# Kernel tuning notes

Hardware: AMD Instinct MI355X
Metric: run time of the kernel (lower is better)

Reference implementation:

```python
import jax, jax.numpy as jnp
import numpy as np

B, N, E = 128, 100, 800          # graphs, nodes/graph, edges/graph
TN, TE = B * N, B * E
NODE_EMB, REL_EMB, H = 128, 256, 256   # hidden_size == relation_emb in CoMPILE
R, DEPTH = 200, 3
EDGE_EMB = 2 * NODE_EMB + REL_EMB      # 512


def _gru_dir(x, h0, w_ih, w_hh, b_ih, b_hh):
    """One direction of a torch-style GRU. x: [B,T,H], h0: [B,H] -> [B,T,H]."""
    def step(h, xt):
        gi = xt @ w_ih.T + b_ih
        gh = h @ w_hh.T + b_hh
        i_r, i_z, i_n = jnp.split(gi, 3, axis=-1)
        h_r, h_z, h_n = jnp.split(gh, 3, axis=-1)
        r = jax.nn.sigmoid(i_r + h_r)
        z = jax.nn.sigmoid(i_z + h_z)
        n = jnp.tanh(i_n + r * h_n)
        hn = (1.0 - z) * n + z * h
        return hn, hn
    _, ys = jax.lax.scan(step, h0, jnp.swapaxes(x, 0, 1))
    return jnp.swapaxes(ys, 0, 1)


def setup_inputs() -> dict:
    key = jax.random.key(0)
    ks = iter(jax.random.split(key, 40))
    def w(shape):
        return jax.random.normal(next(ks), shape, jnp.float32) * 0.05
    inp = {}
    inp["node_feat"] = jax.random.normal(next(ks), (TN, NODE_EMB), jnp.float32)
    inp["rel_emb"] = jax.random.normal(next(ks), (R, REL_EMB), jnp.float32)  # final_relation_embeddings
    # model weights (bias=False everywhere except W_o, linear1, gru)
    inp["W_i_node"] = w((H, NODE_EMB))
    inp["W_i_edge"] = w((H, EDGE_EMB))
    inp["Wa1"] = w((H, 2 * H))          # input_attention1
    inp["Wa2"] = w((1, H))              # input_attention2
    inp["W_h_atom"] = w((DEPTH - 1, H, H))
    inp["W_h_bond"] = w((DEPTH - 1, H, H))
    inp["Wd1"] = w((DEPTH - 1, H, H + REL_EMB))  # Attention1_d
    inp["Wd2"] = w((DEPTH - 1, 1, H))            # Attention2_d
    inp["W_comm"] = w((H, 3 * H))       # communicate_mlp
    inp["gru_bias"] = w((H,))
    inp["w_ih_f"] = w((3 * H, H)); inp["w_hh_f"] = w((3 * H, H))
    inp["b_ih_f"] = w((3 * H,));   inp["b_hh_f"] = w((3 * H,))
    inp["w_ih_b"] = w((3 * H, H)); inp["w_hh_b"] = w((3 * H, H))
    inp["b_ih_b"] = w((3 * H,));   inp["b_hh_b"] = w((3 * H,))
    inp["W_o"] = w((H, 2 * H)); inp["b_o"] = w((H,))
    inp["W_lin1"] = w((1, H)); inp["b_lin1"] = w((1,))
    # graph structure: edges stay inside their own subgraph (block-diagonal batching)
    off = (jnp.arange(B, dtype=jnp.int64)[:, None] * N)
    inp["edge_src"] = (jax.random.randint(next(ks), (B, E), 0, N) + off).reshape(-1)
    inp["edge_dst"] = (jax.random.randint(next(ks), (B, E), 0, N) + off).reshape(-1)
    inp["edge_rel"] = jax.random.randint(next(ks), (TE,), 0, R)
    inp["batch_rel"] = jax.random.randint(next(ks), (B,), 0, R)
    inp["src_node"] = jax.random.randint(next(ks), (B,), 0, N) + jnp.arange(B) * N
    inp["tgt_node"] = jax.random.randint(next(ks), (B,), 0, N) + jnp.arange(B) * N
    return inp


def reference(node_feat, rel_emb, W_i_node, W_i_edge, Wa1, Wa2, W_h_atom, W_h_bond,
              Wd1, Wd2, W_comm, gru_bias, w_ih_f, w_hh_f, b_ih_f, b_hh_f,
              w_ih_b, w_hh_b, b_ih_b, b_hh_b, W_o, b_o, W_lin1, b_lin1,
              edge_src, edge_dst, edge_rel, batch_rel, src_node, tgt_node):
    act = jax.nn.relu  # args.activation = 'ReLU'
    tgt_rel = rel_emb[batch_rel]                              # [B,H] per-query relation
    e_rel = rel_emb[edge_rel]                                 # [TE,H]
    edge_feat = jnp.concatenate([node_feat[edge_src], e_rel, node_feat[edge_dst]], 1)  # [TE,EDGE_EMB]
    input_node = act(node_feat @ W_i_node.T)                  # [TN,H]
    message_node = input_node
    input_edge = act(edge_feat @ W_i_edge.T)                  # [TE,H]
    message_edge = input_edge
    edge_tgt_rel = jnp.repeat(tgt_rel, E, axis=0)             # [TE,H] target relation per edge
    total_source = jnp.repeat(src_node, E)                    # [TE] query head node per edge
    total_target = jnp.repeat(tgt_node, E)
    # input edge attention vs translational query embedding
    g_edge = message_node[total_source] + edge_tgt_rel - message_node[total_target]
    att = jnp.tanh(jnp.concatenate([message_edge, g_edge], 1) @ Wa1.T)
    att = jax.nn.sigmoid(att @ Wa2.T)
    message_edge = message_edge * att
    for d in range(DEPTH - 1):
        # edge->node aggregation (MySpMM with target-side incidence e2n_sp)
        agg = jax.ops.segment_sum(message_edge, edge_dst, num_segments=TN)
        message_node = act((message_node + agg) @ W_h_atom[d].T)
        # node->edge (e2n_sp2^T: gather source-node states per edge)
        message_edge = act(input_edge + message_node[edge_src] @ W_h_bond[d].T)
        att = jnp.tanh(jnp.concatenate([message_edge, edge_tgt_rel], 1) @ Wd1[d].T)
        att = jax.nn.sigmoid(att @ Wd2[d].T)
        message_edge = message_edge * att
    agg = jax.ops.segment_sum(message_edge, edge_dst, num_segments=TN)
    agg2 = jnp.concatenate([agg, message_node, input_node], 1) @ W_comm.T  # [TN,H]
    # BatchGRU: uniform graph sizes -> pad/unpad is a reshape
    msg = act(agg2 + gru_bias).reshape(B, N, H)
    h0 = agg2.reshape(B, N, H).max(axis=1)                    # per-graph max of hidden
    out_f = _gru_dir(msg, h0, w_ih_f, w_hh_f, b_ih_f, b_hh_f)
    out_b = _gru_dir(msg[:, ::-1], h0, w_ih_b, w_hh_b, b_ih_b, b_hh_b)[:, ::-1]
    a_message = act(jnp.concatenate([out_f, out_b], -1).reshape(TN, 2 * H))
    atom_h = act(a_message @ W_o.T + b_o)                     # [TN,H]
    conv = jnp.tanh(atom_h[src_node] + tgt_rel - atom_h[tgt_node])  # [B,H]
    return conv @ W_lin1.T + b_lin1                           # [B,1]
```

## Files before the change

### kernel.cpp

```cpp
#include <hip/hip_runtime.h>
#include <cstddef>

#define Bg 128
#define Nn 100
#define Eg 800
#define TNODE 12800
#define TEDGE 102400
#define HD 256
#define NEMB 128
#define REMB 256

typedef short bf8 __attribute__((ext_vector_type(8)));
typedef short bf4 __attribute__((ext_vector_type(4)));
typedef float f4  __attribute__((ext_vector_type(4)));

__device__ __forceinline__ float relu_(float x){ return x > 0.f ? x : 0.f; }
__device__ __forceinline__ float sigm_(float x){ return 1.f/(1.f + __expf(-x)); }
__device__ __forceinline__ float4 ld4(const float* p){ return *(const float4*)p; }
__device__ __forceinline__ void st4(float* p, float4 v){ *(float4*)p = v; }
__device__ __forceinline__ float4 add4(float4 a, float4 b){
    return float4{a.x+b.x, a.y+b.y, a.z+b.z, a.w+b.w};
}
__device__ __forceinline__ float4 relu4(float4 a){
    return float4{relu_(a.x), relu_(a.y), relu_(a.z), relu_(a.w)};
}
__device__ __forceinline__ short f2bf(float f){
    unsigned u = __float_as_uint(f);
    u += 0x7fff + ((u >> 16) & 1);
    return (short)(u >> 16);
}
__device__ __forceinline__ float bf2f(short s){
    return __uint_as_float(((unsigned)(unsigned short)s) << 16);
}
__device__ __forceinline__ void split4(float4 v, bf4& h, bf4& l){
    h.x = f2bf(v.x); l.x = f2bf(v.x - bf2f(h.x));
    h.y = f2bf(v.y); l.y = f2bf(v.y - bf2f(h.y));
    h.z = f2bf(v.z); l.z = f2bf(v.z - bf2f(h.z));
    h.w = f2bf(v.w); l.w = f2bf(v.w - bf2f(h.w));
}
__device__ __forceinline__ f4 mfma_(bf8 a, bf8 b, f4 c){
    return __builtin_amdgcn_mfma_f32_16x16x32_bf16(a, b, c, 0, 0, 0);
}

enum { A_PLAIN=0, A_ADD=1, A_RELUB=2, A_CLAMP=3, A_CAT3=4, A_CAT2R=5 };
enum { E_STORE=0, E_RELU=1, E_BIAS=2, E_BIASRELU=3 };

template<int AM, int EM>
__global__ __launch_bounds__(256, 2)
void mgemm(const float* __restrict__ A0, const float* __restrict__ A1,
           const float* __restrict__ A2, const float* __restrict__ W,
           const float* __restrict__ bias, float* __restrict__ C,
           int M, int N, int K, int lda, int wld)
{
    __shared__ short Ah[128][40], Al[128][40], Bh[128][40], Bl[128][40];
    const int t  = threadIdx.x;
    const int kc = t & 7, lr = t >> 3;
    const int lane = t & 63, wv = t >> 6;
    const int wm = wv >> 1, wn = wv & 1;
    const int frow = lane & 15, fk = (lane >> 4) * 8;
    const int row0 = blockIdx.y * 128, col0 = blockIdx.x * 128;

    f4 acc[4][4] = {};

    for (int k0 = 0; k0 < K; k0 += 32) {
        const int gk = k0 + kc * 4;
        const int kk = kc * 4;
        #pragma unroll
        for (int ri = 0; ri < 4; ri++) {
            int row = lr + 32 * ri;
            int grow = row0 + row;
            float4 v;
            if (AM == A_PLAIN) {
                v = ld4(A0 + (size_t)grow * lda + gk);
            } else if (AM == A_ADD) {
                v = add4(ld4(A0 + (size_t)grow * lda + gk),
                         ld4(A1 + (size_t)grow * lda + gk));
            } else if (AM == A_RELUB) {
                v = relu4(add4(ld4(A0 + (size_t)grow * lda + gk), ld4(A1 + gk)));
            } else if (AM == A_CLAMP) {
                int cr = grow < M ? grow : M - 1;
                v = ld4(A0 + (size_t)cr * lda + gk);
            } else if (AM == A_CAT3) {
                if (gk < HD)        v = ld4(A0 + (size_t)grow * HD + gk);
                else if (gk < 2*HD) v = ld4(A1 + (size_t)grow * HD + gk - HD);
                else                v = ld4(A2 + (size_t)grow * HD + gk - 2*HD);
            } else {
                v = (gk < HD) ? relu4(ld4(A0 + (size_t)grow * HD + gk))
                              : relu4(ld4(A1 + (size_t)grow * HD + gk - HD));
            }
            bf4 h, l; split4(v, h, l);
            *(bf4*)&Ah[row][kk] = h;
            *(bf4*)&Al[row][kk] = l;
        }
        #pragma unroll
        for (int ri = 0; ri < 4; ri++) {
            int wr = lr + 32 * ri;
            float4 v = ld4(W + (size_t)(col0 + wr) * wld + gk);
            bf4 h, l; split4(v, h, l);
            *(bf4*)&Bh[wr][kk] = h;
            *(bf4*)&Bl[wr][kk] = l;
        }
        __syncthreads();
        bf8 ah[4], al[4], bh[4], bl[4];
        #pragma unroll
        for (int mi = 0; mi < 4; mi++) {
            ah[mi] = *(const bf8*)&Ah[wm*64 + mi*16 + frow][fk];
            al[mi] = *(const bf8*)&Al[wm*64 + mi*16 + frow][fk];
        }
        #pragma unroll
        for (int ni = 0; ni < 4; ni++) {
            bh[ni] = *(const bf8*)&Bh[wn*64 + ni*16 + frow][fk];
            bl[ni] = *(const bf8*)&Bl[wn*64 + ni*16 + frow][fk];
        }
        #pragma unroll
        for (int mi = 0; mi < 4; mi++)
            #pragma unroll
            for (int ni = 0; ni < 4; ni++) {
                acc[mi][ni] = mfma_(ah[mi], bh[ni], acc[mi][ni]);
                acc[mi][ni] = mfma_(ah[mi], bl[ni], acc[mi][ni]);
                acc[mi][ni] = mfma_(al[mi], bh[ni], acc[mi][ni]);
            }
        __syncthreads();
    }
    #pragma unroll
    for (int mi = 0; mi < 4; mi++) {
        #pragma unroll
        for (int ni = 0; ni < 4; ni++) {
            int ccol = col0 + wn*64 + ni*16 + frow;
            int rbase = row0 + wm*64 + mi*16 + (lane >> 4) * 4;
            #pragma unroll
            for (int reg = 0; reg < 4; reg++) {
                float v = acc[mi][ni][reg];
                if (EM == E_BIAS || EM == E_BIASRELU) v += bias[ccol];
                if (EM == E_RELU || EM == E_BIASRELU) v = relu_(v);
                C[(size_t)(rbase + reg) * N + ccol] = v;
            }
        }
    }
}

template<int MODE>
__global__ __launch_bounds__(256, 2)
void mattn(const float* __restrict__ S, const float* __restrict__ Rt,
           const float* __restrict__ D, const float* __restrict__ T0,
           const int* __restrict__ esrc, const int* __restrict__ erel,
           const int* __restrict__ edst,
           const float* __restrict__ W1, const float* __restrict__ W2,
           const float* __restrict__ term, float* __restrict__ sbuf)
{
    __shared__ short Ah[64][40], Al[64][40], Bh[256][40], Bl[256][40];
    __shared__ float partl[4][64];
    __shared__ int isrc[64], irel[64], idst[64];
    const int t = threadIdx.x;
    const int kc = t & 7, lr = t >> 3;
    const int lane = t & 63, wv = t >> 6;
    const int frow = lane & 15, fk = (lane >> 4) * 8;
    const int r0 = blockIdx.x * 64;

    if (t < 64) {
        int e = r0 + t;
        isrc[t] = esrc[e]; irel[t] = erel[e]; idst[t] = edst[e];
    }
    __syncthreads();

    f4 acc[4][4] = {};

    for (int k0 = 0; k0 < HD; k0 += 32) {
        const int gk = k0 + kc * 4;
        const int kk = kc * 4;
        #pragma unroll
        for (int ri = 0; ri < 2; ri++) {
            int row = lr + 32 * ri;
            int s = isrc[row], rl = irel[row], dd = idst[row];
            float4 v = relu4(add4(add4(ld4(S + (size_t)s * HD + gk),
                                       ld4(Rt + (size_t)rl * HD + gk)),
                                  ld4(D + (size_t)dd * HD + gk)));
            if (MODE) v = relu4(add4(v, ld4(T0 + (size_t)s * HD + gk)));
            bf4 h, l; split4(v, h, l);
            *(bf4*)&Ah[row][kk] = h;
            *(bf4*)&Al[row][kk] = l;
        }
        #pragma unroll
        for (int ri = 0; ri < 8; ri++) {
            int wr = lr + 32 * ri;
            float4 v = ld4(W1 + (size_t)wr * 512 + gk);
            bf4 h, l; split4(v, h, l);
            *(bf4*)&Bh[wr][kk] = h;
            *(bf4*)&Bl[wr][kk] = l;
        }
        __syncthreads();
        bf8 ah[4], al[4], bh[4], bl[4];
        #pragma unroll
        for (int mi = 0; mi < 4; mi++) {
            ah[mi] = *(const bf8*)&Ah[mi*16 + frow][fk];
            al[mi] = *(const bf8*)&Al[mi*16 + frow][fk];
        }
        #pragma unroll
        for (int ni = 0; ni < 4; ni++) {
            bh[ni] = *(const bf8*)&Bh[wv*64 + ni*16 + frow][fk];
            bl[ni] = *(const bf8*)&Bl[wv*64 + ni*16 + frow][fk];
        }
        #pragma unroll
        for (int mi = 0; mi < 4; mi++)
            #pragma unroll
            for (int ni = 0; ni < 4; ni++) {
                acc[mi][ni] = mfma_(ah[mi], bh[ni], acc[mi][ni]);
                acc[mi][ni] = mfma_(ah[mi], bl[ni], acc[mi][ni]);
                acc[mi][ni] = mfma_(al[mi], bh[ni], acc[mi][ni]);
            }
        __syncthreads();
    }
    #pragma unroll
    for (int mi = 0; mi < 4; mi++) {
        #pragma unroll
        for (int reg = 0; reg < 4; reg++) {
            int rl = mi*16 + (lane >> 4) * 4 + reg;
            int g = (r0 + rl) / Eg;
            float p = 0.f;
            #pragma unroll
            for (int ni = 0; ni < 4; ni++) {
                int n = wv*64 + ni*16 + frow;
                p += tanhf(acc[mi][ni][reg] + term[g*HD + n]) * W2[n];
            }
            p += __shfl_xor(p, 1); p += __shfl_xor(p, 2);
            p += __shfl_xor(p, 4); p += __shfl_xor(p, 8);
            if (frow == 0) partl[wv][rl] = p;
        }
    }
    __syncthreads();
    if (t < 64) {
        float p = partl[0][t] + partl[1][t] + partl[2][t] + partl[3][t];
        sbuf[r0 + t] = sigm_(p);
    }
}

template<int MODE>
__global__ __launch_bounds__(256)
void agg_gather(const float* __restrict__ S, const float* __restrict__ Rt,
                const float* __restrict__ D, const float* __restrict__ T0,
                const int* __restrict__ esrc, const int* __restrict__ erel,
                const int* __restrict__ rowptr, const int* __restrict__ eidx,
                const float* __restrict__ s, float* __restrict__ agg)
{
    int node = blockIdx.x * 4 + (threadIdx.x >> 6);
    int c = (threadIdx.x & 63) * 4;
    float4 dn = ld4(D + (size_t)node * HD + c);
    float4 acc{0.f, 0.f, 0.f, 0.f};
    int beg = rowptr[node], end = rowptr[node + 1];
    for (int i = beg; i < end; i++) {
        int e = eidx[i];
        int sr = esrc[e], rl = erel[e];
        float4 v = relu4(add4(add4(ld4(S + (size_t)sr * HD + c),
                                   ld4(Rt + (size_t)rl * HD + c)), dn));
        if (MODE) v = relu4(add4(v, ld4(T0 + (size_t)sr * HD + c)));
        float sc = s[e];
        acc.x += v.x * sc; acc.y += v.y * sc;
        acc.z += v.z * sc; acc.w += v.w * sc;
    }
    st4(agg + (size_t)node * HD + c, acc);
}

__global__ void zeroi_kernel(int* __restrict__ p)
{
    p[blockIdx.x * 256 + threadIdx.x] = 0;
}
__global__ void csr_count(const int* __restrict__ dst, int* __restrict__ cnt)
{
    int e = blockIdx.x * 256 + threadIdx.x;
    atomicAdd(&cnt[dst[e]], 1);
}
__global__ void csr_scan(const int* __restrict__ cnt, int* __restrict__ rowptr)
{
    __shared__ int ws[4];
    __shared__ int carry;
    int tid = threadIdx.x;
    if (tid == 0) carry = 0;
    __syncthreads();
    for (int i = 0; i < TNODE; i += 256) {
        int v = cnt[i + tid];
        int x = v;
        #pragma unroll
        for (int off = 1; off < 64; off <<= 1) {
            int y = __shfl_up(x, off);
            if ((tid & 63) >= off) x += y;
        }
        if ((tid & 63) == 63) ws[tid >> 6] = x;
        __syncthreads();
        int add = carry;
        int w = tid >> 6;
        for (int j = 0; j < w; j++) add += ws[j];
        rowptr[i + tid] = add + x - v;
        __syncthreads();
        if (tid == 255) carry = add + x;
        __syncthreads();
    }
    if (tid == 0) rowptr[TNODE] = carry;
}
__global__ void csr_fill(const int* __restrict__ dst, const int* __restrict__ rowptr,
                         int* __restrict__ fillc, int* __restrict__ eidx)
{
    int e = blockIdx.x * 256 + threadIdx.x;
    int d = dst[e];
    int slot = rowptr[d] + atomicAdd(&fillc[d], 1);
    eidx[slot] = e;
}

__global__ __launch_bounds__(256)
void term_kernel(const float* __restrict__ mn, const float* __restrict__ tgt_rel,
                 const float* __restrict__ Wa1, const float* __restrict__ Wd1,
                 const int* __restrict__ srcn, const int* __restrict__ tgtn,
                 float* __restrict__ term)
{
    __shared__ float Gs[HD];
    int b = blockIdx.x % Bg;
    int which = blockIdx.x / Bg;
    int c = threadIdx.x;
    float g;
    if (which == 0)
        g = mn[(size_t)srcn[b]*HD + c] + tgt_rel[b*HD + c] - mn[(size_t)tgtn[b]*HD + c];
    else
        g = tgt_rel[b*HD + c];
    Gs[c] = g;
    __syncthreads();
    const float* W = (which == 0) ? Wa1 : (Wd1 + (size_t)(which-1)*HD*512);
    float p = 0.f;
    for (int k = 0; k < HD; k += 4) {
        float4 w = ld4(W + (size_t)c*512 + 256 + k);
        p = fmaf(Gs[k], w.x, p); p = fmaf(Gs[k+1], w.y, p);
        p = fmaf(Gs[k+2], w.z, p); p = fmaf(Gs[k+3], w.w, p);
    }
    term[(size_t)which*Bg*HD + b*HD + c] = p;
}

__global__ void tgtrel_kernel(const float* __restrict__ rel_emb, const int* __restrict__ batch_rel,
                              float* __restrict__ tgt_rel)
{
    int b = blockIdx.x, c = threadIdx.x;
    tgt_rel[b*HD + c] = rel_emb[(size_t)batch_rel[b]*REMB + c];
}

__global__ void h0_kernel(const float* __restrict__ agg2, float* __restrict__ h0)
{
    int b = blockIdx.x, c = threadIdx.x;
    float m = -1e30f;
    for (int n = 0; n < Nn; n++)
        m = fmaxf(m, agg2[((size_t)b*Nn + n)*HD + c]);
    h0[b*HD + c] = m;
}

__global__ void whbf_kernel(const float* __restrict__ whf, const float* __restrict__ whb,
                            short* __restrict__ whbf)
{
    int idx = blockIdx.x * 256 + threadIdx.x;
    int d = idx / (768*256), rem = idx % (768*256);
    whbf[idx] = f2bf((d ? whb : whf)[rem]);
}

__global__ __launch_bounds__(512, 2)
void gru_seq(const float* __restrict__ gi_f, const float* __restrict__ gi_b,
             const short* __restrict__ whbf,
             const float* __restrict__ bhf, const float* __restrict__ bhb,
             const float* __restrict__ h0,
             float* __restrict__ outf, float* __restrict__ outb)
{
    __shared__ float hsf[16][260];
    __shared__ short hsh[16][264];
    __shared__ short hsl[16][264];
    __shared__ float gates[768][17];
    __shared__ float bsh[768];
    const int blk = blockIdx.x;
    const int d = blk >> 3, grp = blk & 7;
    const int tid = threadIdx.x;
    const int lane = tid & 63, wv = tid >> 6;
    const int f16 = lane & 15;
    const int kb  = (lane >> 4) * 8;

    const short* wp0 = whbf + (size_t)d * 768 * 256;
    const float* gi  = d ? gi_b : gi_f;
    const float* bh  = d ? bhb : bhf;
    float* outp      = d ? outb : outf;

    for (int i = tid; i < 768; i += 512) bsh[i] = bh[i];

    bf8 wreg[6][8];
    #pragma unroll
    for (int j = 0; j < 6; j++) {
        int wr = (wv*6 + j) * 16 + f16;
        const short* wp = wp0 + (size_t)wr * 256 + kb;
        #pragma unroll
        for (int ks = 0; ks < 8; ks++)
            wreg[j][ks] = *(const bf8*)(wp + ks*32);
    }

    const int eseq = tid >> 5, ehb = tid & 31;
    {
        #pragma unroll
        for (int hh = 0; hh < 8; hh++) {
            int h = ehb + hh * 32;
            float v = h0[(size_t)(grp*16 + eseq) * HD + h];
            hsf[eseq][h] = v;
            short hi = f2bf(v);
            hsh[eseq][h] = hi;
            hsl[eseq][h] = f2bf(v - bf2f(hi));
        }
    }
    __syncthreads();

    for (int t = 0; t < Nn; t++) {
        int trow = d ? (Nn - 1 - t) : t;
        float gr[8], gz[8], gn[8];
        {
            size_t girow = ((size_t)(grp*16 + eseq) * Nn + trow) * 768;
            #pragma unroll
            for (int hh = 0; hh < 8; hh++) {
                int h = ehb + hh * 32;
                gr[hh] = gi[girow + h];
                gz[hh] = gi[girow + 256 + h];
                gn[hh] = gi[girow + 512 + h];
            }
        }
        #pragma unroll
        for (int j = 0; j < 6; j++) {
            f4 acc = {};
            #pragma unroll
            for (int ks = 0; ks < 8; ks++) {
                bf8 ahi = *(const bf8*)&hsh[f16][ks*32 + kb];
                bf8 alo = *(const bf8*)&hsl[f16][ks*32 + kb];
                acc = mfma_(ahi, wreg[j][ks], acc);
                acc = mfma_(alo, wreg[j][ks], acc);
            }
            #pragma unroll
            for (int reg = 0; reg < 4; reg++)
                gates[(wv*6 + j)*16 + f16][(lane >> 4)*4 + reg] = acc[reg];
        }
        __syncthreads();
        {
            size_t orow = ((size_t)(grp*16 + eseq) * Nn + trow) * HD;
            #pragma unroll
            for (int hh = 0; hh < 8; hh++) {
                int h = ehb + hh * 32;
                float R  = gates[h][eseq];
                float Z  = gates[256 + h][eseq];
                float NN = gates[512 + h][eseq];
                float hprev = hsf[eseq][h];
                float r = sigm_(gr[hh] + R + bsh[h]);
                float z = sigm_(gz[hh] + Z + bsh[256 + h]);
                float n = tanhf(gn[hh] + r * (NN + bsh[512 + h]));
                float nh = (1.f - z) * n + z * hprev;
                hsf[eseq][h] = nh;
                short hi = f2bf(nh);
                hsh[eseq][h] = hi;
                hsl[eseq][h] = f2bf(nh - bf2f(hi));
                outp[orow + h] = nh;
            }
        }
        __syncthreads();
    }
}

__global__ __launch_bounds__(256)
void final_kernel(const float* __restrict__ atom_h, const float* __restrict__ tgt_rel,
                  const int* __restrict__ srcn, const int* __restrict__ tgtn,
                  const float* __restrict__ Wl, const float* __restrict__ bl,
                  float* __restrict__ out)
{
    __shared__ float red[4];
    int b = blockIdx.x, c = threadIdx.x;
    float v = tanhf(atom_h[(size_t)srcn[b]*HD + c] + tgt_rel[b*HD + c]
                    - atom_h[(size_t)tgtn[b]*HD + c]);
    float p = v * Wl[c];
    #pragma unroll
    for (int off = 1; off < 64; off <<= 1) p += __shfl_xor(p, off);
    int wv = c >> 6;
    if ((c & 63) == 0) red[wv] = p;
    __syncthreads();
    if (c == 0) out[b] = red[0] + red[1] + red[2] + red[3] + bl[0];
}

extern "C" void kernel_launch(void* const* d_in, const int* in_sizes, int n_in,
                              void* d_out, int out_size, void* d_ws, size_t ws_size,
                              hipStream_t stream)
{
    const float* node_feat = (const float*)d_in[0];
    const float* rel_emb   = (const float*)d_in[1];
    const float* W_i_node  = (const float*)d_in[2];
    const float* W_i_edge  = (const float*)d_in[3];
    const float* Wa1       = (const float*)d_in[4];
    const float* Wa2       = (const float*)d_in[5];
    const float* W_h_atom  = (const float*)d_in[6];
    const float* W_h_bond  = (const float*)d_in[7];
    const float* Wd1       = (const float*)d_in[8];
    const float* Wd2       = (const float*)d_in[9];
    const float* W_comm    = (const float*)d_in[10];
    const float* gru_bias  = (const float*)d_in[11];
    const float* w_ih_f    = (const float*)d_in[12];
    const float* w_hh_f    = (const float*)d_in[13];
    const float* b_ih_f    = (const float*)d_in[14];
    const float* b_hh_f    = (const float*)d_in[15];
    const float* w_ih_b    = (const float*)d_in[16];
    const float* w_hh_b    = (const float*)d_in[17];
    const float* b_ih_b    = (const float*)d_in[18];
    const float* b_hh_b    = (const float*)d_in[19];
    const float* W_o       = (const float*)d_in[20];
    const float* b_o       = (const float*)d_in[21];
    const float* W_lin1    = (const float*)d_in[22];
    const float* b_lin1    = (const float*)d_in[23];
    const int* edge_src  = (const int*)d_in[24];
    const int* edge_dst  = (const int*)d_in[25];
    const int* edge_rel  = (const int*)d_in[26];
    const int* batch_rel = (const int*)d_in[27];
    const int* src_node  = (const int*)d_in[28];
    const int* tgt_node  = (const int*)d_in[29];
    float* out = (float*)d_out;

    float* ws = (float*)d_ws;
    size_t off = 0;
    auto alloc = [&](size_t n){ float* p = ws + off; off += n; return p; };
    float* tgt_rel    = alloc((size_t)Bg*HD);
    float* term       = alloc((size_t)3*Bg*HD);
    float* input_node = alloc((size_t)TNODE*HD);
    float* mn_a       = alloc((size_t)TNODE*HD);
    float* mn_b       = alloc((size_t)TNODE*HD);
    float* agg        = alloc((size_t)TNODE*HD);
    float* h0v        = alloc((size_t)Bg*HD);
    short* whbf       = (short*)alloc((size_t)2*768*256/2);
    float* sbuf       = alloc((size_t)TEDGE);
    int*   cnt        = (int*)alloc((size_t)TNODE);
    int*   fillc      = (int*)alloc((size_t)TNODE);
    int*   rowptr     = (int*)alloc((size_t)TNODE + 256);
    int*   eidx       = (int*)alloc((size_t)TEDGE);
    float* Sbuf       = alloc((size_t)TNODE*HD);
    float* Dbuf       = alloc((size_t)TNODE*HD);
    float* Rbuf       = alloc((size_t)256*HD);
    float* gi_f       = alloc((size_t)TNODE*768);
    float* gi_b       = alloc((size_t)TNODE*768);
    float* out_f      = alloc((size_t)TNODE*HD);
    float* out_b      = alloc((size_t)TNODE*HD);
    float* agg2   = mn_a;
    float* atom_h = input_node;

    tgtrel_kernel<<<Bg, 256, 0, stream>>>(rel_emb, batch_rel, tgt_rel);
    whbf_kernel<<<1536, 256, 0, stream>>>(w_hh_f, w_hh_b, whbf);

    zeroi_kernel<<<2*TNODE/256, 256, 0, stream>>>(cnt);
    csr_count<<<TEDGE/256, 256, 0, stream>>>(edge_dst, cnt);
    csr_scan<<<1, 256, 0, stream>>>(cnt, rowptr);
    csr_fill<<<TEDGE/256, 256, 0, stream>>>(edge_dst, rowptr, fillc, eidx);

    mgemm<A_PLAIN, E_RELU><<<dim3(HD/128, TNODE/128), 256, 0, stream>>>(
        node_feat, nullptr, nullptr, W_i_node, nullptr, input_node,
        TNODE, HD, NEMB, NEMB, NEMB);

    mgemm<A_PLAIN, E_STORE><<<dim3(HD/128, TNODE/128), 256, 0, stream>>>(
        node_feat, nullptr, nullptr, W_i_edge + 0, nullptr, Sbuf,
        TNODE, HD, NEMB, NEMB, 512);
    mgemm<A_PLAIN, E_STORE><<<dim3(HD/128, TNODE/128), 256, 0, stream>>>(
        node_feat, nullptr, nullptr, W_i_edge + 384, nullptr, Dbuf,
        TNODE, HD, NEMB, NEMB, 512);
    mgemm<A_CLAMP, E_STORE><<<dim3(HD/128, 2), 256, 0, stream>>>(
        rel_emb, nullptr, nullptr, W_i_edge + 128, nullptr, Rbuf,
        200, HD, REMB, REMB, 512);

    term_kernel<<<3*Bg, 256, 0, stream>>>(input_node, tgt_rel, Wa1, Wd1,
                                          src_node, tgt_node, term);

    mattn<0><<<TEDGE/64, 256, 0, stream>>>(Sbuf, Rbuf, Dbuf, Sbuf,
        edge_src, edge_rel, edge_dst, Wa1, Wa2, term, sbuf);
    agg_gather<0><<<TNODE/4, 256, 0, stream>>>(Sbuf, Rbuf, Dbuf, Sbuf,
        edge_src, edge_rel, rowptr, eidx, sbuf, agg);

    const float* mn_cur = input_node;
    float* bufs[2] = {mn_a, mn_b};
    for (int d = 0; d < 2; d++) {
        float* mn_next = bufs[d];
        float* tmp     = bufs[1-d];
        mgemm<A_ADD, E_RELU><<<dim3(2, TNODE/128), 256, 0, stream>>>(
            mn_cur, agg, nullptr, W_h_atom + (size_t)d*HD*HD, nullptr, mn_next,
            TNODE, HD, HD, HD, HD);
        mgemm<A_PLAIN, E_STORE><<<dim3(2, TNODE/128), 256, 0, stream>>>(
            mn_next, nullptr, nullptr, W_h_bond + (size_t)d*HD*HD, nullptr, tmp,
            TNODE, HD, HD, HD, HD);
        mattn<1><<<TEDGE/64, 256, 0, stream>>>(Sbuf, Rbuf, Dbuf, tmp,
            edge_src, edge_rel, edge_dst, Wd1 + (size_t)d*HD*512,
            Wd2 + (size_t)d*HD, term + (size_t)(1+d)*Bg*HD, sbuf);
        agg_gather<1><<<TNODE/4, 256, 0, stream>>>(Sbuf, Rbuf, Dbuf, tmp,
            edge_src, edge_rel, rowptr, eidx, sbuf, agg);
        mn_cur = mn_next;
    }

    mgemm<A_CAT3, E_STORE><<<dim3(2, TNODE/128), 256, 0, stream>>>(
        agg, (const float*)mn_cur, input_node, W_comm, nullptr, agg2,
        TNODE, HD, 3*HD, 0, 3*HD);

    h0_kernel<<<Bg, 256, 0, stream>>>(agg2, h0v);

    mgemm<A_RELUB, E_BIAS><<<dim3(768/128, TNODE/128), 256, 0, stream>>>(
        agg2, gru_bias, nullptr, w_ih_f, b_ih_f, gi_f,
        TNODE, 768, HD, HD, HD);
    mgemm<A_RELUB, E_BIAS><<<dim3(768/128, TNODE/128), 256, 0, stream>>>(
        agg2, gru_bias, nullptr, w_ih_b, b_ih_b, gi_b,
        TNODE, 768, HD, HD, HD);

    gru_seq<<<16, 512, 0, stream>>>(gi_f, gi_b, whbf, b_hh_f, b_hh_b, h0v,
                                    out_f, out_b);

    mgemm<A_CAT2R, E_BIASRELU><<<dim3(2, TNODE/128), 256, 0, stream>>>(
        out_f, out_b, nullptr, W_o, b_o, atom_h,
        TNODE, HD, 2*HD, 0, 2*HD);

    final_kernel<<<Bg, 256, 0, stream>>>(atom_h, tgt_rel, src_node, tgt_node,
                                         W_lin1, b_lin1, out);
}
```

Measured before the change: 1.478 ms.

## Restructure GRU recurrence to 4 waves with more register-held weights and folded biases

The sequential GRU kernel now runs 256 threads per block instead of 512, so each wave keeps 12 weight tiles in registers and interleaves four independent MFMA accumulators to hide MFMA latency. The r/z hidden biases are folded into the input-gate GEMM bias through a small new kernel, and the n-gate hidden bias is kept in registers, which removes the shared bias table. Input-gate loads move after the barrier and become float4 vector loads, as do the output stores. The trade-off is fewer waves per block, higher register pressure, and less latency hiding for the global gate loads.

```diff
diff --git a/kernel.cpp b/kernel.cpp
--- a/kernel.cpp
+++ b/kernel.cpp
@@ -356,7 +356,18 @@
     whbf[idx] = f2bf((d ? whb : whf)[rem]);
 }
 
-__global__ __launch_bounds__(512, 2)
+__global__ void biascomb_kernel(const float* __restrict__ bihf, const float* __restrict__ bhhf,
+                                const float* __restrict__ bihb, const float* __restrict__ bhhb,
+                                float* __restrict__ bc)
+{
+    int i = blockIdx.x * 256 + threadIdx.x;
+    int d = i / 768, r = i % 768;
+    const float* bi = d ? bihb : bihf;
+    const float* bhh = d ? bhhb : bhhf;
+    bc[i] = bi[r] + (r < 512 ? bhh[r] : 0.f);
+}
+
+__global__ __launch_bounds__(256, 1)
 void gru_seq(const float* __restrict__ gi_f, const float* __restrict__ gi_b,
              const short* __restrict__ whbf,
              const float* __restrict__ bhf, const float* __restrict__ bhb,
@@ -367,7 +378,6 @@
     __shared__ short hsh[16][264];
     __shared__ short hsl[16][264];
     __shared__ float gates[768][17];
-    __shared__ float bsh[768];
     const int blk = blockIdx.x;
     const int d = blk >> 3, grp = blk & 7;
     const int tid = threadIdx.x;
@@ -380,23 +390,26 @@
     const float* bh  = d ? bhb : bhf;
     float* outp      = d ? outb : outf;
 
-    for (int i = tid; i < 768; i += 512) bsh[i] = bh[i];
-
-    bf8 wreg[6][8];
+    bf8 wreg[12][8];
     #pragma unroll
-    for (int j = 0; j < 6; j++) {
-        int wr = (wv*6 + j) * 16 + f16;
+    for (int j = 0; j < 12; j++) {
+        int wr = (wv*12 + j) * 16 + f16;
         const short* wp = wp0 + (size_t)wr * 256 + kb;
         #pragma unroll
         for (int ks = 0; ks < 8; ks++)
             wreg[j][ks] = *(const bf8*)(wp + ks*32);
     }
 
-    const int eseq = tid >> 5, ehb = tid & 31;
+    const int eseq = tid >> 4;
+    const int eh0  = (tid & 15) * 16;
+    float bhn[16];
+    #pragma unroll
+    for (int hh = 0; hh < 16; hh++) bhn[hh] = bh[512 + eh0 + hh];
+
     {
         #pragma unroll
-        for (int hh = 0; hh < 8; hh++) {
-            int h = ehb + hh * 32;
+        for (int hh = 0; hh < 16; hh++) {
+            int h = eh0 + hh;
             float v = h0[(size_t)(grp*16 + eseq) * HD + h];
             hsf[eseq][h] = v;
             short hi = f2bf(v);
@@ -408,50 +421,64 @@
 
     for (int t = 0; t < Nn; t++) {
         int trow = d ? (Nn - 1 - t) : t;
-        float gr[8], gz[8], gn[8];
-        {
-            size_t girow = ((size_t)(grp*16 + eseq) * Nn + trow) * 768;
-            #pragma unroll
-            for (int hh = 0; hh < 8; hh++) {
-                int h = ehb + hh * 32;
-                gr[hh] = gi[girow + h];
-                gz[hh] = gi[girow + 256 + h];
-                gn[hh] = gi[girow + 512 + h];
-            }
-        }
-        #pragma unroll
-        for (int j = 0; j < 6; j++) {
-            f4 acc = {};
+        #pragma unroll
+        for (int g = 0; g < 3; g++) {
+            f4 acc0 = {}, acc1 = {}, acc2 = {}, acc3 = {};
             #pragma unroll
             for (int ks = 0; ks < 8; ks++) {
                 bf8 ahi = *(const bf8*)&hsh[f16][ks*32 + kb];
                 bf8 alo = *(const bf8*)&hsl[f16][ks*32 + kb];
-                acc = mfma_(ahi, wreg[j][ks], acc);
-                acc = mfma_(alo, wreg[j][ks], acc);
-            }
+                acc0 = mfma_(ahi, wreg[g*4+0][ks], acc0);
+                acc1 = mfma_(ahi, wreg[g*4+1][ks], acc1);
+                acc2 = mfma_(ahi, wreg[g*4+2][ks], acc2);
+                acc3 = mfma_(ahi, wreg[g*4+3][ks], acc3);
+                acc0 = mfma_(alo, wreg[g*4+0][ks], acc0);
+                acc1 = mfma_(alo, wreg[g*4+1][ks], acc1);
+                acc2 = mfma_(alo, wreg[g*4+2][ks], acc2);
+                acc3 = mfma_(alo, wreg[g*4+3][ks], acc3);
+            }
+            int rb = (wv*12 + g*4) * 16 + f16;
+            int cb = (lane >> 4) * 4;
             #pragma unroll
-            for (int reg = 0; reg < 4; reg++)
-                gates[(wv*6 + j)*16 + f16][(lane >> 4)*4 + reg] = acc[reg];
+            for (int reg = 0; reg < 4; reg++) {
+                gates[rb +  0][cb + reg] = acc0[reg];
+                gates[rb + 16][cb + reg] = acc1[reg];
+                gates[rb + 32][cb + reg] = acc2[reg];
+                gates[rb + 48][cb + reg] = acc3[reg];
+            }
         }
         __syncthreads();
         {
-            size_t orow = ((size_t)(grp*16 + eseq) * Nn + trow) * HD;
+            size_t girow = ((size_t)(grp*16 + eseq) * Nn + trow) * 768;
+            size_t orow  = ((size_t)(grp*16 + eseq) * Nn + trow) * HD;
             #pragma unroll
-            for (int hh = 0; hh < 8; hh++) {
-                int h = ehb + hh * 32;
-                float R  = gates[h][eseq];
-                float Z  = gates[256 + h][eseq];
-                float NN = gates[512 + h][eseq];
-                float hprev = hsf[eseq][h];
-                float r = sigm_(gr[hh] + R + bsh[h]);
-                float z = sigm_(gz[hh] + Z + bsh[256 + h]);
-                float n = tanhf(gn[hh] + r * (NN + bsh[512 + h]));
-                float nh = (1.f - z) * n + z * hprev;
-                hsf[eseq][h] = nh;
-                short hi = f2bf(nh);
-                hsh[eseq][h] = hi;
-                hsl[eseq][h] = f2bf(nh - bf2f(hi));
-                outp[orow + h] = nh;
+            for (int c2 = 0; c2 < 4; c2++) {
+                int hb = eh0 + c2*4;
+                float4 g_r = ld4(gi + girow + hb);
+                float4 g_z = ld4(gi + girow + 256 + hb);
+                float4 g_n = ld4(gi + girow + 512 + hb);
+                float4 onew;
+                #pragma unroll
+                for (int e = 0; e < 4; e++) {
+                    int h = hb + e;
+                    float R  = gates[h][eseq];
+                    float Z  = gates[256 + h][eseq];
+                    float NN = gates[512 + h][eseq];
+                    float hprev = hsf[eseq][h];
+                    float gre = ((const float*)&g_r)[e];
+                    float gze = ((const float*)&g_z)[e];
+                    float gne = ((const float*)&g_n)[e];
+                    float r = sigm_(gre + R);
+                    float z = sigm_(gze + Z);
+                    float n = tanhf(gne + r * (NN + bhn[c2*4 + e]));
+                    float nh = (1.f - z) * n + z * hprev;
+                    hsf[eseq][h] = nh;
+                    short hi = f2bf(nh);
+                    hsh[eseq][h] = hi;
+                    hsl[eseq][h] = f2bf(nh - bf2f(hi));
+                    ((float*)&onew)[e] = nh;
+                }
+                st4(outp + orow + hb, onew);
             }
         }
         __syncthreads();
@@ -524,6 +551,7 @@
     float* agg        = alloc((size_t)TNODE*HD);
     float* h0v        = alloc((size_t)Bg*HD);
     short* whbf       = (short*)alloc((size_t)2*768*256/2);
+    float* bcomb      = alloc((size_t)2*768);
     float* sbuf       = alloc((size_t)TEDGE);
     int*   cnt        = (int*)alloc((size_t)TNODE);
     int*   fillc      = (int*)alloc((size_t)TNODE);
@@ -541,6 +569,7 @@
 
     tgtrel_kernel<<<Bg, 256, 0, stream>>>(rel_emb, batch_rel, tgt_rel);
     whbf_kernel<<<1536, 256, 0, stream>>>(w_hh_f, w_hh_b, whbf);
+    biascomb_kernel<<<6, 256, 0, stream>>>(b_ih_f, b_hh_f, b_ih_b, b_hh_b, bcomb);
 
     zeroi_kernel<<<2*TNODE/256, 256, 0, stream>>>(cnt);
     csr_count<<<TEDGE/256, 256, 0, stream>>>(edge_dst, cnt);
@@ -595,13 +624,13 @@
     h0_kernel<<<Bg, 256, 0, stream>>>(agg2, h0v);
 
     mgemm<A_RELUB, E_BIAS><<<dim3(768/128, TNODE/128), 256, 0, stream>>>(
-        agg2, gru_bias, nullptr, w_ih_f, b_ih_f, gi_f,
+        agg2, gru_bias, nullptr, w_ih_f, bcomb, gi_f,
         TNODE, 768, HD, HD, HD);
     mgemm<A_RELUB, E_BIAS><<<dim3(768/128, TNODE/128), 256, 0, stream>>>(
-        agg2, gru_bias, nullptr, w_ih_b, b_ih_b, gi_b,
+        agg2, gru_bias, nullptr, w_ih_b, bcomb + 768, gi_b,
         TNODE, 768, HD, HD, HD);
 
-    gru_seq<<<16, 512, 0, stream>>>(gi_f, gi_b, whbf, b_hh_f, b_hh_b, h0v,
+    gru_seq<<<16, 256, 0, stream>>>(gi_f, gi_b, whbf, b_hh_f, b_hh_b, h0v,
                                     out_f, out_b);
 
     mgemm<A_CAT2R, E_BIASRELU><<<dim3(2, TNODE/128), 256, 0, stream>>>(
```

Result: slower. 1.799 ms (+21.8%).

## Fold GRU hidden biases into input GEMM and halve register-resident recurrent weights

Applied to the files above, without the earlier changes.

Precomputes combined r/z biases (b_ih + b_hh) and passes them to the input-projection GEMM epilogue, so the sequential GRU kernel no longer stages biases in shared memory and keeps only the n-gate hidden bias in registers. It also keeps just half of the recurrent weight fragments in registers and reloads the other half from global memory (L2/L1) on every timestep. This lowers register pressure in the latency-bound recurrent loop, but adds global loads to each step of the serial chain.

```diff
diff --git a/kernel.cpp b/kernel.cpp
--- a/kernel.cpp
+++ b/kernel.cpp
@@ -356,6 +356,17 @@
     whbf[idx] = f2bf((d ? whb : whf)[rem]);
 }
 
+__global__ void biascomb_kernel(const float* __restrict__ bihf, const float* __restrict__ bhhf,
+                                const float* __restrict__ bihb, const float* __restrict__ bhhb,
+                                float* __restrict__ bc)
+{
+    int i = blockIdx.x * 256 + threadIdx.x;
+    int d = i / 768, r = i % 768;
+    const float* bi = d ? bihb : bihf;
+    const float* bhh = d ? bhhb : bhhf;
+    bc[i] = bi[r] + (r < 512 ? bhh[r] : 0.f);
+}
+
 __global__ __launch_bounds__(512, 2)
 void gru_seq(const float* __restrict__ gi_f, const float* __restrict__ gi_b,
              const short* __restrict__ whbf,
@@ -367,7 +378,6 @@
     __shared__ short hsh[16][264];
     __shared__ short hsl[16][264];
     __shared__ float gates[768][17];
-    __shared__ float bsh[768];
     const int blk = blockIdx.x;
     const int d = blk >> 3, grp = blk & 7;
     const int tid = threadIdx.x;
@@ -380,19 +390,21 @@
     const float* bh  = d ? bhb : bhf;
     float* outp      = d ? outb : outf;
 
-    for (int i = tid; i < 768; i += 512) bsh[i] = bh[i];
-
-    bf8 wreg[6][8];
+    bf8 wregA[3][8];
     #pragma unroll
-    for (int j = 0; j < 6; j++) {
+    for (int j = 0; j < 3; j++) {
         int wr = (wv*6 + j) * 16 + f16;
         const short* wp = wp0 + (size_t)wr * 256 + kb;
         #pragma unroll
         for (int ks = 0; ks < 8; ks++)
-            wreg[j][ks] = *(const bf8*)(wp + ks*32);
+            wregA[j][ks] = *(const bf8*)(wp + ks*32);
     }
 
     const int eseq = tid >> 5, ehb = tid & 31;
+    float bhn[8];
+    #pragma unroll
+    for (int hh = 0; hh < 8; hh++) bhn[hh] = bh[512 + ehb + hh * 32];
+
     {
         #pragma unroll
         for (int hh = 0; hh < 8; hh++) {
@@ -421,13 +433,15 @@
         }
         #pragma unroll
         for (int j = 0; j < 6; j++) {
+            const short* wp = wp0 + (size_t)((wv*6 + j) * 16 + f16) * 256 + kb;
             f4 acc = {};
             #pragma unroll
             for (int ks = 0; ks < 8; ks++) {
                 bf8 ahi = *(const bf8*)&hsh[f16][ks*32 + kb];
                 bf8 alo = *(const bf8*)&hsl[f16][ks*32 + kb];
-                acc = mfma_(ahi, wreg[j][ks], acc);
-                acc = mfma_(alo, wreg[j][ks], acc);
+                bf8 b = (j < 3) ? wregA[j][ks] : *(const bf8*)(wp + ks*32);
+                acc = mfma_(ahi, b, acc);
+                acc = mfma_(alo, b, acc);
             }
             #pragma unroll
             for (int reg = 0; reg < 4; reg++)
@@ -443,9 +457,9 @@
                 float Z  = gates[256 + h][eseq];
                 float NN = gates[512 + h][eseq];
                 float hprev = hsf[eseq][h];
-                float r = sigm_(gr[hh] + R + bsh[h]);
-                float z = sigm_(gz[hh] + Z + bsh[256 + h]);
-                float n = tanhf(gn[hh] + r * (NN + bsh[512 + h]));
+                float r = sigm_(gr[hh] + R);
+                float z = sigm_(gz[hh] + Z);
+                float n = tanhf(gn[hh] + r * (NN + bhn[hh]));
                 float nh = (1.f - z) * n + z * hprev;
                 hsf[eseq][h] = nh;
                 short hi = f2bf(nh);
@@ -524,6 +538,7 @@
     float* agg        = alloc((size_t)TNODE*HD);
     float* h0v        = alloc((size_t)Bg*HD);
     short* whbf       = (short*)alloc((size_t)2*768*256/2);
+    float* bcomb      = alloc((size_t)2*768);
     float* sbuf       = alloc((size_t)TEDGE);
     int*   cnt        = (int*)alloc((size_t)TNODE);
     int*   fillc      = (int*)alloc((size_t)TNODE);
@@ -541,6 +556,7 @@
 
     tgtrel_kernel<<<Bg, 256, 0, stream>>>(rel_emb, batch_rel, tgt_rel);
     whbf_kernel<<<1536, 256, 0, stream>>>(w_hh_f, w_hh_b, whbf);
+    biascomb_kernel<<<6, 256, 0, stream>>>(b_ih_f, b_hh_f, b_ih_b, b_hh_b, bcomb);
 
     zeroi_kernel<<<2*TNODE/256, 256, 0, stream>>>(cnt);
     csr_count<<<TEDGE/256, 256, 0, stream>>>(edge_dst, cnt);
@@ -595,10 +611,10 @@
     h0_kernel<<<Bg, 256, 0, stream>>>(agg2, h0v);
 
     mgemm<A_RELUB, E_BIAS><<<dim3(768/128, TNODE/128), 256, 0, stream>>>(
-        agg2, gru_bias, nullptr, w_ih_f, b_ih_f, gi_f,
+        agg2, gru_bias, nullptr, w_ih_f, bcomb, gi_f,
         TNODE, 768, HD, HD, HD);
     mgemm<A_RELUB, E_BIAS><<<dim3(768/128, TNODE/128), 256, 0, stream>>>(
-        agg2, gru_bias, nullptr, w_ih_b, b_ih_b, gi_b,
+        agg2, gru_bias, nullptr, w_ih_b, bcomb + 768, gi_b,
         TNODE, 768, HD, HD, HD);
 
     gru_seq<<<16, 512, 0, stream>>>(gi_f, gi_b, whbf, b_hh_f, b_hh_b, h0v,
```

Result: slower. 1.545 ms (+4.6%).
